# Optimization experiments

Hardware: AMD Instinct MI355X
Metric: run time of the kernel (lower is better)

The kernel has to match this reference:

```python
import jax, jax.numpy as jnp
import numpy as np

NS_ITERS = 15
EPS = 1e-6


def _sqrtm(x):
    """Newton-Schulz matrix square root, 15 fixed iterations (Lin & Maji)."""
    dim = x.shape[0]
    norm = jnp.linalg.norm(x)  # Frobenius norm
    Y = x / norm
    I = jnp.eye(dim, dtype=x.dtype)
    Z = I
    for _ in range(NS_ITERS):
        T = 0.5 * (3.0 * I - Z @ Y)
        Y = Y @ T
        Z = T @ Z
    return Y * jnp.sqrt(norm)


def _gram(X):
    a, b = X.shape
    return (X @ X.T + EPS * jnp.eye(a, dtype=X.dtype)) / b


def setup_inputs() -> dict:
    key = jax.random.key(0)
    k1, k2 = jax.random.split(key)
    inp = jax.random.normal(k1, (1, 512, 256, 256), dtype=jnp.float32)
    tgt = jax.random.normal(k2, (1, 512, 256, 256), dtype=jnp.float32)
    return {"input": inp, "target_feature": tgt}


def reference(input, target_feature):
    a, b, c, d = input.shape
    n = a * b
    # --- target statistics (precomputed in __init__ of the torch module) ---
    Xt = target_feature.reshape(n, c * d)
    Mt = Xt.mean(axis=1)                     # [n]
    Gt = _gram(Xt - Mt[:, None])             # [n, n]
    sqrt_Gt = _sqrtm(Gt)                     # [n, n]
    # --- current statistics ---
    X = input.reshape(n, c * d)
    M = X.mean(axis=1)
    G = _gram(X - M[:, None])
    sqrt_G = _sqrtm(G)
    # mse(reduction='sum') on means + Bures/Wasserstein SPD distance
    loss = jnp.sum((M - Mt) ** 2)
    loss = loss + jnp.trace(G + Gt) - 2.0 * jnp.trace(sqrt_G @ sqrt_Gt)
    return loss / b
```

## Files before the change

kernel.cpp:

```cpp
#include <hip/hip_runtime.h>
#include <math.h>

#define KDIM 65536
#define MATF 262144
#define EPSG 1e-6

using bf16x8 = __attribute__((ext_vector_type(8))) __bf16;
using f32x4  = __attribute__((ext_vector_type(4))) float;


__global__ __launch_bounds__(256) void k_means(const float* __restrict__ X,
                                               const float* __restrict__ Xt,
                                               float* __restrict__ M) {
  const int row = blockIdx.x, inp = blockIdx.y;
  const float4* p = (const float4*)((inp ? Xt : X) + (size_t)row * KDIM);
  double s = 0.0;
  for (int i = threadIdx.x; i < KDIM / 4; i += 256) {
    float4 v = p[i];
    s += (double)v.x + (double)v.y + (double)v.z + (double)v.w;
  }
  __shared__ double sm[256];
  sm[threadIdx.x] = s;
  __syncthreads();
  for (int o = 128; o > 0; o >>= 1) {
    if (threadIdx.x < o) sm[threadIdx.x] += sm[threadIdx.x + o];
    __syncthreads();
  }
  if (threadIdx.x == 0) M[inp * 512 + row] = (float)(sm[0] * (1.0 / KDIM));
}

__device__ __forceinline__ void cvt8(float4 a, float4 b, bf16x8& hi, bf16x8& lo) {
  float f[8] = {a.x, a.y, a.z, a.w, b.x, b.y, b.z, b.w};
#pragma unroll
  for (int e = 0; e < 8; ++e) {
    __bf16 h = (__bf16)f[e];
    hi[e] = h;
    lo[e] = (__bf16)(f[e] - (float)h);
  }
}

__global__ __launch_bounds__(256, 2) void k_gram(const float* __restrict__ X,
                                                 const float* __restrict__ Xt,
                                                 float* __restrict__ Gp, int nk) {
  int rem = blockIdx.x, ti = 0;
  while (rem >= 4 - ti) { rem -= 4 - ti; ++ti; }
  const int tj = ti + rem;
  const int chunk = blockIdx.y, inp = blockIdx.z;
  const int chunkv = KDIM / nk;
  const float* __restrict__ A = inp ? Xt : X;
  float* __restrict__ C = Gp + ((size_t)(inp * nk + chunk)) * MATF;
  const bool diag = (ti == tj);

  __shared__ bf16x8 AhV[512], AlV[512], BhV[512], BlV[512];

  const int t = threadIdx.x;
  const int srow = t & 127, skh = t >> 7;
  const int sbase = ((srow >> 4) << 6) + (skh << 5) + (srow & 15);

  const float* pa = A + (size_t)(ti * 128 + srow) * KDIM + (size_t)chunk * chunkv + skh * 16;
  const float* pb = A + (size_t)(tj * 128 + srow) * KDIM + (size_t)chunk * chunkv + skh * 16;

  const int wave = t >> 6, lane = t & 63;
  const int wy = (wave >> 1) * 64, wx = (wave & 1) * 64;

  f32x4 acc[4][4];
#pragma unroll
  for (int i = 0; i < 4; ++i)
#pragma unroll
    for (int j = 0; j < 4; ++j) acc[i][j] = (f32x4){0.f, 0.f, 0.f, 0.f};

  float4 ra0 = *(const float4*)(pa);
  float4 ra1 = *(const float4*)(pa + 4);
  float4 ra2 = *(const float4*)(pa + 8);
  float4 ra3 = *(const float4*)(pa + 12);
  float4 rb0 = {}, rb1 = {}, rb2 = {}, rb3 = {};
  if (!diag) {
    rb0 = *(const float4*)(pb);
    rb1 = *(const float4*)(pb + 4);
    rb2 = *(const float4*)(pb + 8);
    rb3 = *(const float4*)(pb + 12);
  }

  for (int ks = 0; ks < chunkv; ks += 32) {
    {
      bf16x8 h, l;
      cvt8(ra0, ra1, h, l); AhV[sbase] = h; AlV[sbase] = l;
      cvt8(ra2, ra3, h, l); AhV[sbase + 16] = h; AlV[sbase + 16] = l;
      if (!diag) {
        cvt8(rb0, rb1, h, l); BhV[sbase] = h; BlV[sbase] = l;
        cvt8(rb2, rb3, h, l); BhV[sbase + 16] = h; BlV[sbase + 16] = l;
      }
    }
    __syncthreads();
    if (ks + 32 < chunkv) {
      ra0 = *(const float4*)(pa + ks + 32);
      ra1 = *(const float4*)(pa + ks + 36);
      ra2 = *(const float4*)(pa + ks + 40);
      ra3 = *(const float4*)(pa + ks + 44);
      if (!diag) {
        rb0 = *(const float4*)(pb + ks + 32);
        rb1 = *(const float4*)(pb + ks + 36);
        rb2 = *(const float4*)(pb + ks + 40);
        rb3 = *(const float4*)(pb + ks + 44);
      }
    }
    const bf16x8* __restrict__ Bh = diag ? AhV : BhV;
    const bf16x8* __restrict__ Bl = diag ? AlV : BlV;
    bf16x8 ah[4], al[4], bh[4], bl[4];
#pragma unroll
    for (int g = 0; g < 4; ++g) {
      ah[g] = AhV[((wave >> 1) * 4 + g) * 64 + lane];
      al[g] = AlV[((wave >> 1) * 4 + g) * 64 + lane];
      bh[g] = Bh[((wave & 1) * 4 + g) * 64 + lane];
      bl[g] = Bl[((wave & 1) * 4 + g) * 64 + lane];
    }
#pragma unroll
    for (int i = 0; i < 4; ++i)
#pragma unroll
      for (int j = 0; j < 4; ++j) {
        acc[i][j] = __builtin_amdgcn_mfma_f32_16x16x32_bf16(ah[i], bh[j], acc[i][j], 0, 0, 0);
        acc[i][j] = __builtin_amdgcn_mfma_f32_16x16x32_bf16(al[i], bh[j], acc[i][j], 0, 0, 0);
        acc[i][j] = __builtin_amdgcn_mfma_f32_16x16x32_bf16(ah[i], bl[j], acc[i][j], 0, 0, 0);
      }
    __syncthreads();
  }
  const int r4 = (lane >> 4) * 4, fc = lane & 15;
#pragma unroll
  for (int i = 0; i < 4; ++i) {
    const int grow = ti * 128 + wy + i * 16 + r4;
#pragma unroll
    for (int j = 0; j < 4; ++j) {
      const int gcol = tj * 128 + wx + j * 16 + fc;
#pragma unroll
      for (int r = 0; r < 4; ++r)
        C[(size_t)(grow + r) * 512 + gcol] = acc[i][j][r];
    }
  }
}

__device__ __forceinline__ void gbar(unsigned* cnt, unsigned target) {
  __syncthreads();
  if (threadIdx.x == 0) {
    __threadfence();
    atomicAdd(cnt, 1u);
    unsigned long long t0 = __builtin_amdgcn_s_memrealtime();
    while (__hip_atomic_load(cnt, __ATOMIC_RELAXED, __HIP_MEMORY_SCOPE_AGENT) < target) {
      __builtin_amdgcn_s_sleep(16);
      if (__builtin_amdgcn_s_memrealtime() - t0 > 2000000ull) break;
    }
    __threadfence();
  }
  __syncthreads();
}

__device__ __forceinline__ void tri8(int x, int& ti, int& tj) {
  int rem = x, i = 0;
  while (rem >= 8 - i) { rem -= 8 - i; ++i; }
  ti = i; tj = i + rem;
}

__device__ __forceinline__ void gemm64(const float* __restrict__ A,
                                       const float* __restrict__ B,
                                       const float* __restrict__ E,
                                       float* __restrict__ C,
                                       int ti, int tj, int mode,
                                       bf16x8* AhV, bf16x8* AlV,
                                       bf16x8* BhV, bf16x8* BlV) {
  const int t = threadIdx.x;
  const int srow = t & 63, sko = t >> 6;
  const int sslot = ((srow >> 4) << 6) + (sko << 4) + (srow & 15);

  const float* pa = A + (size_t)(ti * 64 + srow) * 512 + sko * 8;
  const float* pb = B + (size_t)(tj * 64 + srow) * 512 + sko * 8;

  const int wave = t >> 6, lane = t & 63;
  const int wy = (wave >> 1) * 32, wx = (wave & 1) * 32;

  f32x4 acc[2][2];
#pragma unroll
  for (int i = 0; i < 2; ++i)
#pragma unroll
    for (int j = 0; j < 2; ++j) acc[i][j] = (f32x4){0.f, 0.f, 0.f, 0.f};

  float4 ra0 = *(const float4*)(pa), ra1 = *(const float4*)(pa + 4);
  float4 rb0 = *(const float4*)(pb), rb1 = *(const float4*)(pb + 4);

  for (int ks = 0; ks < 512; ks += 32) {
    {
      bf16x8 h, l;
      cvt8(ra0, ra1, h, l); AhV[sslot] = h; AlV[sslot] = l;
      cvt8(rb0, rb1, h, l); BhV[sslot] = h; BlV[sslot] = l;
    }
    __syncthreads();
    if (ks + 32 < 512) {
      ra0 = *(const float4*)(pa + ks + 32); ra1 = *(const float4*)(pa + ks + 36);
      rb0 = *(const float4*)(pb + ks + 32); rb1 = *(const float4*)(pb + ks + 36);
    }
    bf16x8 ah[2], al[2], bh[2], bl[2];
#pragma unroll
    for (int g = 0; g < 2; ++g) {
      ah[g] = AhV[((wy >> 4) + g) * 64 + lane];
      al[g] = AlV[((wy >> 4) + g) * 64 + lane];
      bh[g] = BhV[((wx >> 4) + g) * 64 + lane];
      bl[g] = BlV[((wx >> 4) + g) * 64 + lane];
    }
#pragma unroll
    for (int i = 0; i < 2; ++i)
#pragma unroll
      for (int j = 0; j < 2; ++j) {
        acc[i][j] = __builtin_amdgcn_mfma_f32_16x16x32_bf16(ah[i], bh[j], acc[i][j], 0, 0, 0);
        acc[i][j] = __builtin_amdgcn_mfma_f32_16x16x32_bf16(al[i], bh[j], acc[i][j], 0, 0, 0);
        acc[i][j] = __builtin_amdgcn_mfma_f32_16x16x32_bf16(ah[i], bl[j], acc[i][j], 0, 0, 0);
      }
    __syncthreads();
  }

  const int r4 = (lane >> 4) * 4, fc = lane & 15;
#pragma unroll
  for (int i = 0; i < 2; ++i) {
    const int grow = ti * 64 + wy + i * 16 + r4;
#pragma unroll
    for (int j = 0; j < 2; ++j) {
      const int gcol = tj * 64 + wx + j * 16 + fc;
      float v[4];
#pragma unroll
      for (int r = 0; r < 4; ++r) v[r] = acc[i][j][r];
      if (mode) {
#pragma unroll
        for (int r = 0; r < 4; ++r)
          v[r] = 1.5f * E[(size_t)(grow + r) * 512 + gcol] - 0.5f * v[r];
      }
#pragma unroll
      for (int r = 0; r < 4; ++r) C[(size_t)(grow + r) * 512 + gcol] = v[r];
      if (ti != tj) {
        float4 mv = make_float4(v[0], v[1], v[2], v[3]);
        *(float4*)&C[(size_t)gcol * 512 + grow] = mv;
      }
    }
  }
}

__global__ __launch_bounds__(256, 2) void k_all(const float* Gp,
                                                const float* __restrict__ M,
                                                float* __restrict__ Gm,
                                                double* __restrict__ S,
                                                unsigned* __restrict__ bar,
                                                float* big,
                                                float* __restrict__ out, int nk) {
  __shared__ bf16x8 AhV[256], AlV[256], BhV[256], BlV[256];
  __shared__ double red[256];
  __shared__ float s_nrm[2];

  const int t = threadIdx.x;
  const int b = blockIdx.x;
  const int gsz = gridDim.x;
  unsigned tgt = 0;

  float* Ya = big;
  float* Yb = big + 2 * (size_t)MATF;
  float* Za = big + 4 * (size_t)MATF;
  float* Zb = big + 6 * (size_t)MATF;
  float* W  = big + 8 * (size_t)MATF;

  {
    double n2[2] = {0.0, 0.0}, trc[2] = {0.0, 0.0};
    for (int e = b * 256 + t; e < 2 * MATF; e += gsz * 256) {
      const int inp = e >> 18, idx = e & (MATF - 1);
      const int i = idx >> 9, j = idx & 511;
      if (i <= j) {
        double sum = 0.0;
        const float* p = Gp + (size_t)inp * nk * MATF + idx;
        for (int c = 0; c < nk; ++c) sum += (double)p[(size_t)c * MATF];
        sum -= 65536.0 * (double)M[inp * 512 + i] * (double)M[inp * 512 + j];
        if (i == j) sum += EPSG;
        float v = (float)(sum * (1.0 / 65536.0));
        Gm[e] = v;
        if (i < j) { Gm[((size_t)inp << 18) + j * 512 + i] = v; n2[inp] += 2.0 * (double)v * (double)v; }
        else       { n2[inp] += (double)v * (double)v; trc[inp] += (double)v; }
      }
    }
#pragma unroll
    for (int inp = 0; inp < 2; ++inp) {
      red[t] = n2[inp]; __syncthreads();
      for (int o = 128; o > 0; o >>= 1) { if (t < o) red[t] += red[t + o]; __syncthreads(); }
      if (t == 0) atomicAdd(&S[inp], red[0]);
      __syncthreads();
      red[t] = trc[inp]; __syncthreads();
      for (int o = 128; o > 0; o >>= 1) { if (t < o) red[t] += red[t + o]; __syncthreads(); }
      if (t == 0) atomicAdd(&S[2 + inp], red[0]);
      __syncthreads();
    }
  }
  gbar(bar, tgt += gsz);

  {
    if (t < 2)
      s_nrm[t] = (float)sqrt(__hip_atomic_load(&S[t], __ATOMIC_RELAXED, __HIP_MEMORY_SCOPE_AGENT));
    __syncthreads();
    for (int e = b * 256 + t; e < 2 * MATF; e += gsz * 256) {
      const int inp = e >> 18, idx = e & (MATF - 1);
      const float y = Gm[e] / s_nrm[inp];
      Ya[e] = y;
      Za[e] = ((idx >> 9) == (idx & 511)) ? (1.5f - 0.5f * y) : (-0.5f * y);
    }
  }
  gbar(bar, tgt += gsz);

  for (int job = b; job < 72; job += gsz) {
    const int mat = job >= 36;
    int ti, tj; tri8(job - mat * 36, ti, tj);
    const float* a = Ya + (size_t)mat * MATF;
    gemm64(a, a, a, Yb + (size_t)mat * MATF, ti, tj, 1, AhV, AlV, BhV, BlV);
  }
  gbar(bar, tgt += gsz);

  float *Y = Yb, *Z = Za, *Yn = Ya, *Zn = Zb;
  for (int it = 1; it < 15; ++it) {
    for (int job = b; job < 72; job += gsz) {
      const int mat = job >= 36;
      int ti, tj; tri8(job - mat * 36, ti, tj);
      gemm64(Z + (size_t)mat * MATF, Y + (size_t)mat * MATF, nullptr,
             W + (size_t)mat * MATF, ti, tj, 0, AhV, AlV, BhV, BlV);
    }
    gbar(bar, tgt += gsz);
    for (int job = b; job < 144; job += gsz) {
      if (job < 72) {
        const int mat = job >= 36;
        int ti, tj; tri8(job - mat * 36, ti, tj);
        gemm64(Y + (size_t)mat * MATF, W + (size_t)mat * MATF, Y + (size_t)mat * MATF,
               Yn + (size_t)mat * MATF, ti, tj, 1, AhV, AlV, BhV, BlV);
      } else {
        const int jb = job - 72;
        const int mat = jb >= 36;
        int ti, tj; tri8(jb - mat * 36, ti, tj);
        gemm64(W + (size_t)mat * MATF, Z + (size_t)mat * MATF, Z + (size_t)mat * MATF,
               Zn + (size_t)mat * MATF, ti, tj, 1, AhV, AlV, BhV, BlV);
      }
    }
    gbar(bar, tgt += gsz);
    float* tmp;
    tmp = Y; Y = Yn; Yn = tmp;
    tmp = Z; Z = Zn; Zn = tmp;
  }

  {
    double s = 0.0;
    for (int id = b * 256 + t; id < MATF; id += gsz * 256) {
      const int i = id >> 9, j = id & 511;
      s += (double)Y[id] * (double)Y[MATF + j * 512 + i];
    }
    red[t] = s;
    __syncthreads();
    for (int o = 128; o > 0; o >>= 1) {
      if (t < o) red[t] += red[t + o];
      __syncthreads();
    }
    if (t == 0) atomicAdd(&S[4], red[0]);
  }
  gbar(bar, tgt += gsz);

  if (b == 0) {
    double s = 0.0;
    for (int i = t; i < 512; i += 256) {
      double d = (double)M[i] - (double)M[512 + i];
      s += d * d;
    }
    red[t] = s;
    __syncthreads();
    for (int o = 128; o > 0; o >>= 1) {
      if (t < o) red[t] += red[t + o];
      __syncthreads();
    }
    if (t == 0) {
      double s0 = __hip_atomic_load(&S[0], __ATOMIC_RELAXED, __HIP_MEMORY_SCOPE_AGENT);
      double s1 = __hip_atomic_load(&S[1], __ATOMIC_RELAXED, __HIP_MEMORY_SCOPE_AGENT);
      double s2 = __hip_atomic_load(&S[2], __ATOMIC_RELAXED, __HIP_MEMORY_SCOPE_AGENT);
      double s3 = __hip_atomic_load(&S[3], __ATOMIC_RELAXED, __HIP_MEMORY_SCOPE_AGENT);
      double s4 = __hip_atomic_load(&S[4], __ATOMIC_RELAXED, __HIP_MEMORY_SCOPE_AGENT);
      double scale = sqrt(sqrt(s0) * sqrt(s1));
      double loss = red[0] + s2 + s3 - 2.0 * scale * s4;
      out[0] = (float)(loss / 512.0);
    }
  }
}

extern "C" void kernel_launch(void* const* d_in, const int* in_sizes, int n_in,
                              void* d_out, int out_size, void* d_ws, size_t ws_size,
                              hipStream_t stream) {
  const float* X = (const float*)d_in[0];
  const float* Xt = (const float*)d_in[1];
  char* wsb = (char*)d_ws;
  unsigned* bar = (unsigned*)wsb;
  double* S = (double*)(wsb + 4096);
  float* Mv = (float*)(wsb + 4224);
  float* G = (float*)(wsb + 16384);
  float* big = (float*)(wsb + 16384 + 2 * (size_t)MATF * 4);

  const size_t need32 = 16384 + 2 * (size_t)MATF * 4 + 2 * 32 * (size_t)MATF * 4;
  const int nk = (ws_size >= need32) ? 32 : 16;

  static int s_grid = 0;
  if (s_grid == 0) {
    int dev = 0;
    hipGetDevice(&dev);
    int ncu = 0;
    hipDeviceGetAttribute(&ncu, hipDeviceAttributeMultiprocessorCount, dev);
    int maxb = 0;
    hipOccupancyMaxActiveBlocksPerMultiprocessor(&maxb, k_all, 256, 0);
    if (ncu <= 0) ncu = 64;
    if (maxb <= 0) maxb = 1;
    long cap = (long)ncu * maxb;
    s_grid = (cap < 256) ? (int)cap : 256;
    if (s_grid < 1) s_grid = 1;
  }

  hipMemsetAsync(wsb, 0, 4224, stream);
  k_means<<<dim3(512, 2), 256, 0, stream>>>(X, Xt, Mv);
  k_gram<<<dim3(10, nk, 2), 256, 0, stream>>>(X, Xt, big, nk);
  k_all<<<dim3(s_grid), 256, 0, stream>>>(big, Mv, G, S, bar, big,
                                          (float*)d_out, nk);
}
```

Before: 1.612 ms.

## Replace grid-barrier thread fences with agent-scope relaxed atomic loads/stores

Removes the __threadfence calls from the software grid barrier and replaces them with an s_waitcnt plus relaxed agent-scope atomic increments. To keep cross-block visibility without the fences, every global load and store of the shared matrices in the persistent kernel is turned into a scalar agent-scope atomic access, which bypasses non-coherent caching. The barrier spin sleep is also shortened. This trades cheaper barriers for losing the float4 vectorised loads and stores in the GEMM tiles and adds per-element atomic traffic.

```diff
diff --git a/kernel.cpp b/kernel.cpp
--- a/kernel.cpp
+++ b/kernel.cpp
@@ -8,6 +8,16 @@
 using bf16x8 = __attribute__((ext_vector_type(8))) __bf16;
 using f32x4  = __attribute__((ext_vector_type(4))) float;
 
+
+__device__ __forceinline__ float aload(const float* p) {
+  return __hip_atomic_load(p, __ATOMIC_RELAXED, __HIP_MEMORY_SCOPE_AGENT);
+}
+__device__ __forceinline__ void astore(float* p, float v) {
+  __hip_atomic_store(p, v, __ATOMIC_RELAXED, __HIP_MEMORY_SCOPE_AGENT);
+}
+__device__ __forceinline__ float4 aload4(const float* p) {
+  return make_float4(aload(p), aload(p + 1), aload(p + 2), aload(p + 3));
+}
 
 __global__ __launch_bounds__(256) void k_means(const float* __restrict__ X,
                                                const float* __restrict__ Xt,
@@ -139,16 +149,15 @@
 }
 
 __device__ __forceinline__ void gbar(unsigned* cnt, unsigned target) {
+  asm volatile("s_waitcnt vmcnt(0)" ::: "memory");
   __syncthreads();
   if (threadIdx.x == 0) {
-    __threadfence();
-    atomicAdd(cnt, 1u);
+    __hip_atomic_fetch_add(cnt, 1u, __ATOMIC_RELAXED, __HIP_MEMORY_SCOPE_AGENT);
     unsigned long long t0 = __builtin_amdgcn_s_memrealtime();
     while (__hip_atomic_load(cnt, __ATOMIC_RELAXED, __HIP_MEMORY_SCOPE_AGENT) < target) {
-      __builtin_amdgcn_s_sleep(16);
+      __builtin_amdgcn_s_sleep(8);
       if (__builtin_amdgcn_s_memrealtime() - t0 > 2000000ull) break;
     }
-    __threadfence();
   }
   __syncthreads();
 }
@@ -159,10 +168,8 @@
   ti = i; tj = i + rem;
 }
 
-__device__ __forceinline__ void gemm64(const float* __restrict__ A,
-                                       const float* __restrict__ B,
-                                       const float* __restrict__ E,
-                                       float* __restrict__ C,
+__device__ __forceinline__ void gemm64(const float* A, const float* B,
+                                       const float* E, float* C,
                                        int ti, int tj, int mode,
                                        bf16x8* AhV, bf16x8* AlV,
                                        bf16x8* BhV, bf16x8* BlV) {
@@ -182,8 +189,8 @@
 #pragma unroll
     for (int j = 0; j < 2; ++j) acc[i][j] = (f32x4){0.f, 0.f, 0.f, 0.f};
 
-  float4 ra0 = *(const float4*)(pa), ra1 = *(const float4*)(pa + 4);
-  float4 rb0 = *(const float4*)(pb), rb1 = *(const float4*)(pb + 4);
+  float4 ra0 = aload4(pa), ra1 = aload4(pa + 4);
+  float4 rb0 = aload4(pb), rb1 = aload4(pb + 4);
 
   for (int ks = 0; ks < 512; ks += 32) {
     {
@@ -193,8 +200,8 @@
     }
     __syncthreads();
     if (ks + 32 < 512) {
-      ra0 = *(const float4*)(pa + ks + 32); ra1 = *(const float4*)(pa + ks + 36);
-      rb0 = *(const float4*)(pb + ks + 32); rb1 = *(const float4*)(pb + ks + 36);
+      ra0 = aload4(pa + ks + 32); ra1 = aload4(pa + ks + 36);
+      rb0 = aload4(pb + ks + 32); rb1 = aload4(pb + ks + 36);
     }
     bf16x8 ah[2], al[2], bh[2], bl[2];
 #pragma unroll
@@ -228,13 +235,12 @@
       if (mode) {
 #pragma unroll
         for (int r = 0; r < 4; ++r)
-          v[r] = 1.5f * E[(size_t)(grow + r) * 512 + gcol] - 0.5f * v[r];
-      }
-#pragma unroll
-      for (int r = 0; r < 4; ++r) C[(size_t)(grow + r) * 512 + gcol] = v[r];
-      if (ti != tj) {
-        float4 mv = make_float4(v[0], v[1], v[2], v[3]);
-        *(float4*)&C[(size_t)gcol * 512 + grow] = mv;
+          v[r] = 1.5f * aload(E + (size_t)(grow + r) * 512 + gcol) - 0.5f * v[r];
+      }
+#pragma unroll
+      for (int r = 0; r < 4; ++r) {
+        astore(C + (size_t)(grow + r) * 512 + gcol, v[r]);
+        if (ti != tj) astore(C + (size_t)gcol * 512 + grow + r, v[r]);
       }
     }
   }
@@ -274,8 +280,8 @@
         sum -= 65536.0 * (double)M[inp * 512 + i] * (double)M[inp * 512 + j];
         if (i == j) sum += EPSG;
         float v = (float)(sum * (1.0 / 65536.0));
-        Gm[e] = v;
-        if (i < j) { Gm[((size_t)inp << 18) + j * 512 + i] = v; n2[inp] += 2.0 * (double)v * (double)v; }
+        astore(&Gm[e], v);
+        if (i < j) { astore(&Gm[((size_t)inp << 18) + j * 512 + i], v); n2[inp] += 2.0 * (double)v * (double)v; }
         else       { n2[inp] += (double)v * (double)v; trc[inp] += (double)v; }
       }
     }
@@ -299,9 +305,9 @@
     __syncthreads();
     for (int e = b * 256 + t; e < 2 * MATF; e += gsz * 256) {
       const int inp = e >> 18, idx = e & (MATF - 1);
-      const float y = Gm[e] / s_nrm[inp];
-      Ya[e] = y;
-      Za[e] = ((idx >> 9) == (idx & 511)) ? (1.5f - 0.5f * y) : (-0.5f * y);
+      const float y = aload(&Gm[e]) / s_nrm[inp];
+      astore(&Ya[e], y);
+      astore(&Za[e], ((idx >> 9) == (idx & 511)) ? (1.5f - 0.5f * y) : (-0.5f * y));
     }
   }
   gbar(bar, tgt += gsz);
@@ -347,7 +353,7 @@
     double s = 0.0;
     for (int id = b * 256 + t; id < MATF; id += gsz * 256) {
       const int i = id >> 9, j = id & 511;
-      s += (double)Y[id] * (double)Y[MATF + j * 512 + i];
+      s += (double)aload(&Y[id]) * (double)aload(&Y[MATF + j * 512 + i]);
     }
     red[t] = s;
     __syncthreads();
```

Result: slower. 2.301 ms (+42.8%).
